# Kernel optimization log

Measured on AMD Instinct MI355X. Metric: run time of the kernel, lower is better.

Reference implementation:

```python
import jax, jax.numpy as jnp
import numpy as np

B, N, ENC, DEC, ATT = 32, 4096, 1024, 512, 512


def setup_inputs() -> dict:
    key = jax.random.key(0)
    ks = jax.random.split(key, 8)
    s_enc = 1.0 / np.sqrt(ENC)
    s_dec = 1.0 / np.sqrt(DEC)
    s_att = 1.0 / np.sqrt(ATT)
    return {
        "encoder_out": jax.random.normal(ks[0], (B, N, ENC), jnp.float32),
        "decoder_hidden": jax.random.normal(ks[1], (B, DEC), jnp.float32),
        "W_enc": jax.random.uniform(ks[2], (ENC, ATT), jnp.float32, -s_enc, s_enc),
        "b_enc": jax.random.uniform(ks[3], (ATT,), jnp.float32, -s_enc, s_enc),
        "W_dec": jax.random.uniform(ks[4], (DEC, ATT), jnp.float32, -s_dec, s_dec),
        "b_dec": jax.random.uniform(ks[5], (ATT,), jnp.float32, -s_dec, s_dec),
        "w_full": jax.random.uniform(ks[6], (ATT,), jnp.float32, -s_att, s_att),
        "b_full": jax.random.uniform(ks[7], (), jnp.float32, -s_att, s_att),
    }


def reference(encoder_out, decoder_hidden, W_enc, b_enc, W_dec, b_dec, w_full, b_full):
    # att1: [B, N, ATT]; att2: [B, 1, ATT]
    att1 = jnp.einsum('bne,ea->bna', encoder_out, W_enc) + b_enc
    att2 = (decoder_hidden @ W_dec + b_dec)[:, None, :]
    att = jax.nn.relu(att1 + att2)
    e = jnp.einsum('bna,a->bn', att, w_full) + b_full  # [B, N]
    alpha = jax.nn.softmax(e, axis=1)
    awe = jnp.einsum('bne,bn->be', encoder_out, alpha)  # weighted encoding [B, ENC]
    return awe, alpha
```

## Files before the change

kernel.cpp:

```cpp
#include <hip/hip_runtime.h>

#define B_ 32
#define N_ 4096
#define ENC_ 1024
#define DEC_ 512
#define ATT_ 512

typedef __attribute__((ext_vector_type(8))) short short8;
typedef __attribute__((ext_vector_type(4))) float f32x4;

__device__ __forceinline__ short f2bf(float f) {
  union { float f; unsigned u; } x; x.f = f;
  unsigned r = (x.u + 0x7FFFu + ((x.u >> 16) & 1u)) >> 16;
  return (short)r;
}

__device__ __forceinline__ void lds_barrier() {
  asm volatile("s_waitcnt lgkmcnt(0)" ::: "memory");
  __builtin_amdgcn_s_barrier();
  asm volatile("" ::: "memory");
}

extern "C" __global__ void __launch_bounds__(256) prep_kernel(
    const float* __restrict__ dh, const float* __restrict__ W_dec,
    const float* __restrict__ b_dec, const float* __restrict__ b_enc,
    const float* __restrict__ W_enc,
    float* __restrict__ att2, short* __restrict__ Wfrag)
{
  if (blockIdx.x < B_) {
    __shared__ float dhs[DEC_];
    int b = blockIdx.x;
    for (int i = threadIdx.x; i < DEC_; i += 256) dhs[i] = dh[b * DEC_ + i];
    __syncthreads();
    for (int a = threadIdx.x; a < ATT_; a += 256) {
      float s = b_dec[a] + b_enc[a];
      for (int k = 0; k < DEC_; ++k) s += dhs[k] * W_dec[k * ATT_ + a];
      att2[b * ATT_ + a] = s;
    }
  } else {
    int idx = (blockIdx.x - B_) * 256 + threadIdx.x;
    int l = idx & 63;
    int g = (idx >> 6) & 31;
    int c = idx >> 11;
    int col = c * 16 + (l & 15);
    int kb = g * 32 + (l >> 4) * 8;
    short8 p;
#pragma unroll
    for (int j = 0; j < 8; ++j) p[j] = f2bf(W_enc[(kb + j) * ATT_ + col]);
    *(short8*)(Wfrag + ((long)idx << 3)) = p;
  }
}

extern "C" __global__ void __launch_bounds__(256, 2) gemm_e_kernel(
    const float* __restrict__ enc, const short* __restrict__ Wfrag,
    const float* __restrict__ att2, const float* __restrict__ w_full,
    float* __restrict__ e_part)
{
  __shared__ __align__(16) short As[2][64 * 64];
  __shared__ float e_red[64][4];

  const int tid = threadIdx.x;
  const int lane = tid & 63;
  const int w = tid >> 6;
  const int blk = blockIdx.x;
  const int g16 = blk >> 4;
  const int h = (blk >> 3) & 1;
  const int p = g16 * 8 + (blk & 7);
  const int b = p >> 6;
  const int n0 = (p & 63) * 64;

  const int arow = tid >> 2;
  const int akc = tid & 3;
  const float* aptr = enc + ((long)(b * N_ + n0 + arow)) * ENC_ + akc * 16;
  const int awb0 = (arow * 128 + akc * 32) ^ ((arow & 7) << 4);
  const int awb1 = (arow * 128 + akc * 32 + 16) ^ ((arow & 7) << 4);

  int arbyte[4][2];
#pragma unroll
  for (int r = 0; r < 4; ++r) {
    int rr = r * 16 + (lane & 15);
#pragma unroll
    for (int s = 0; s < 2; ++s)
      arbyte[r][s] =
          (rr * 128 + (lane >> 4) * 16 + s * 64) ^ ((rr & 7) << 4);
  }

  const short* bptr = Wfrag + (long)(h * 16 + w * 4) * 16384 + lane * 8;

  f32x4 acc[4][4] = {};
  short8 bfgA[4], bfgB[4];
  f32x4 pA[4];

  {
    f32x4 v0 = *(const f32x4*)(aptr);
    f32x4 v1 = *(const f32x4*)(aptr + 4);
    f32x4 v2 = *(const f32x4*)(aptr + 8);
    f32x4 v3 = *(const f32x4*)(aptr + 12);
    short8 q0, q1;
#pragma unroll
    for (int j = 0; j < 4; ++j) {
      q0[j] = f2bf(v0[j]); q0[j + 4] = f2bf(v1[j]);
      q1[j] = f2bf(v2[j]); q1[j + 4] = f2bf(v3[j]);
    }
    *(short8*)((char*)As[0] + awb0) = q0;
    *(short8*)((char*)As[0] + awb1) = q1;
  }
#pragma unroll
  for (int cc = 0; cc < 4; ++cc)
    bfgA[cc] = *(const short8*)(bptr + cc * 16384);
  lds_barrier();

#pragma unroll
  for (int t = 0; t < 16; ++t) {
    const int cur = t & 1;
    if (t + 1 < 16) {
#pragma unroll
      for (int i = 0; i < 4; ++i)
        pA[i] = *(const f32x4*)(aptr + (t + 1) * 64 + i * 4);
    }
    {
#pragma unroll
      for (int cc = 0; cc < 4; ++cc)
        bfgB[cc] = *(const short8*)(bptr + cc * 16384 + (2 * t + 1) * 512);
      short8 af[4];
#pragma unroll
      for (int r = 0; r < 4; ++r)
        af[r] = *(const short8*)((const char*)As[cur] + arbyte[r][0]);
      __builtin_amdgcn_s_setprio(1);
#pragma unroll
      for (int cc = 0; cc < 4; ++cc)
#pragma unroll
        for (int r = 0; r < 4; ++r)
          acc[r][cc] = __builtin_amdgcn_mfma_f32_16x16x32_bf16(
              af[r], bfgA[cc], acc[r][cc], 0, 0, 0);
      __builtin_amdgcn_s_setprio(0);
    }
    {
      if (2 * t + 2 < 32) {
#pragma unroll
        for (int cc = 0; cc < 4; ++cc)
          bfgA[cc] = *(const short8*)(bptr + cc * 16384 + (2 * t + 2) * 512);
      }
      short8 af[4];
#pragma unroll
      for (int r = 0; r < 4; ++r)
        af[r] = *(const short8*)((const char*)As[cur] + arbyte[r][1]);
      __builtin_amdgcn_s_setprio(1);
#pragma unroll
      for (int cc = 0; cc < 4; ++cc)
#pragma unroll
        for (int r = 0; r < 4; ++r)
          acc[r][cc] = __builtin_amdgcn_mfma_f32_16x16x32_bf16(
              af[r], bfgB[cc], acc[r][cc], 0, 0, 0);
      __builtin_amdgcn_s_setprio(0);
    }
    if (t + 1 < 16) {
      short8 q0, q1;
#pragma unroll
      for (int j = 0; j < 4; ++j) {
        q0[j] = f2bf(pA[0][j]); q0[j + 4] = f2bf(pA[1][j]);
        q1[j] = f2bf(pA[2][j]); q1[j + 4] = f2bf(pA[3][j]);
      }
      *(short8*)((char*)As[cur ^ 1] + awb0) = q0;
      *(short8*)((char*)As[cur ^ 1] + awb1) = q1;
      lds_barrier();
    }
  }

  const int lq = lane >> 4, lr = lane & 15;
  float at2v[4], wv[4];
#pragma unroll
  for (int c = 0; c < 4; ++c) {
    int col = h * 256 + w * 64 + c * 16 + lr;
    at2v[c] = att2[b * ATT_ + col];
    wv[c] = w_full[col];
  }
#pragma unroll
  for (int r = 0; r < 4; ++r) {
#pragma unroll
    for (int j = 0; j < 4; ++j) {
      float s = 0.f;
#pragma unroll
      for (int c = 0; c < 4; ++c)
        s += fmaxf(acc[r][c][j] + at2v[c], 0.f) * wv[c];
      s += __shfl_xor(s, 1); s += __shfl_xor(s, 2);
      s += __shfl_xor(s, 4); s += __shfl_xor(s, 8);
      if (lr == 0) e_red[r * 16 + lq * 4 + j][w] = s;
    }
  }
  __syncthreads();
  if (tid < 64) {
    float ev = e_red[tid][0] + e_red[tid][1] + e_red[tid][2] + e_red[tid][3];
    e_part[(long)h * (B_ * N_) + b * N_ + n0 + tid] = ev;
  }
}

extern "C" __global__ void __launch_bounds__(256) softmax_kernel(
    const float* __restrict__ e, float* __restrict__ alpha)
{
  int b = blockIdx.x, tid = threadIdx.x;
  float v[16];
  float m = -1e30f;
#pragma unroll
  for (int i = 0; i < 16; ++i) {
    int idx = b * N_ + i * 256 + tid;
    v[i] = e[idx] + e[B_ * N_ + idx];
    m = fmaxf(m, v[i]);
  }
  for (int off = 1; off < 64; off <<= 1) m = fmaxf(m, __shfl_xor(m, off));
  __shared__ float redm[4];
  if ((tid & 63) == 0) redm[tid >> 6] = m;
  __syncthreads();
  m = fmaxf(fmaxf(redm[0], redm[1]), fmaxf(redm[2], redm[3]));
  float s = 0.f;
#pragma unroll
  for (int i = 0; i < 16; ++i) { v[i] = expf(v[i] - m); s += v[i]; }
  for (int off = 1; off < 64; off <<= 1) s += __shfl_xor(s, off);
  __shared__ float reds[4];
  if ((tid & 63) == 0) reds[tid >> 6] = s;
  __syncthreads();
  s = reds[0] + reds[1] + reds[2] + reds[3];
  float inv = 1.0f / s;
#pragma unroll
  for (int i = 0; i < 16; ++i) alpha[b * N_ + i * 256 + tid] = v[i] * inv;
}

extern "C" __global__ void __launch_bounds__(256) awe_part_kernel(
    const float* __restrict__ enc, const float* __restrict__ alpha,
    float* __restrict__ part)
{
  __shared__ float als[256];
  __shared__ f32x4 red[256];
  int bi = blockIdx.x;
  int b = bi & 31, cchunk = (bi >> 5) & 3, nchunk = bi >> 7;
  int t = threadIdx.x;
  int n0 = nchunk * 256;
  als[t] = alpha[b * N_ + n0 + t];
  __syncthreads();
  int tcol = t & 63, tn = t >> 6;
  const float* base = enc + (long)b * N_ * ENC_ + (long)n0 * ENC_ +
                      cchunk * 256 + tcol * 4;
  f32x4 acc = {};
  for (int i = tn; i < 256; i += 4) {
    f32x4 vv = *(const f32x4*)(base + (long)i * ENC_);
    acc += als[i] * vv;
  }
  red[t] = acc;
  __syncthreads();
  if (t < 64) {
    f32x4 s = red[t] + red[t + 64] + red[t + 128] + red[t + 192];
    *(f32x4*)(&part[(long)nchunk * 32768 + b * 1024 + cchunk * 256 + t * 4]) = s;
  }
}

extern "C" __global__ void __launch_bounds__(256) awe_reduce_kernel(
    const float* __restrict__ part, float* __restrict__ awe)
{
  int i = blockIdx.x * 256 + threadIdx.x;
  float s = 0.f;
#pragma unroll
  for (int p = 0; p < 16; ++p) s += part[(long)p * 32768 + i];
  awe[i] = s;
}

extern "C" void kernel_launch(void* const* d_in, const int* in_sizes, int n_in,
                              void* d_out, int out_size, void* d_ws, size_t ws_size,
                              hipStream_t stream) {
  const float* enc    = (const float*)d_in[0];
  const float* dh     = (const float*)d_in[1];
  const float* W_enc  = (const float*)d_in[2];
  const float* b_enc  = (const float*)d_in[3];
  const float* W_dec  = (const float*)d_in[4];
  const float* b_dec  = (const float*)d_in[5];
  const float* w_full = (const float*)d_in[6];
  float* out = (float*)d_out;

  char* ws = (char*)d_ws;
  float* att2  = (float*)ws;
  short* Wfrag = (short*)(ws + 65536);
  float* e_buf = (float*)(ws + 65536 + 1048576);
  float* part  = (float*)(ws + 65536 + 1048576 + 1048576);

  hipLaunchKernelGGL(prep_kernel, dim3(B_ + 256), dim3(256), 0, stream,
                     dh, W_dec, b_dec, b_enc, W_enc, att2, Wfrag);
  hipLaunchKernelGGL(gemm_e_kernel, dim3(4096), dim3(256), 0, stream,
                     enc, Wfrag, att2, w_full, e_buf);
  hipLaunchKernelGGL(softmax_kernel, dim3(B_), dim3(256), 0, stream,
                     e_buf, out + B_ * ENC_);
  hipLaunchKernelGGL(awe_part_kernel, dim3(2048), dim3(256), 0, stream,
                     enc, out + B_ * ENC_, part);
  hipLaunchKernelGGL(awe_reduce_kernel, dim3(128), dim3(256), 0, stream,
                     part, out);
}
```

Baseline: 328.2 us.

## Stage encoder tiles via direct global-to-LDS loads and convert to bf16 on read

Replaces the register-staged A-tile path (global load, bf16 convert, LDS store) with global_load_lds DMA of raw fp32 tiles into a swizzled LDS layout, converting to bf16 when fragments are read. It also drops the B-fragment register double-buffering, loading B per k-step instead, and raises the occupancy hint from 2 to 3 blocks per CU. The aim is to cut VGPR pressure and the instruction overhead of staging. In exchange LDS use doubles to 32 KB per buffer pair, which may limit occupancy, and conversion work is repeated on every read.

```diff
diff --git a/kernel.cpp b/kernel.cpp
--- a/kernel.cpp
+++ b/kernel.cpp
@@ -15,10 +15,10 @@
   return (short)r;
 }
 
-__device__ __forceinline__ void lds_barrier() {
-  asm volatile("s_waitcnt lgkmcnt(0)" ::: "memory");
-  __builtin_amdgcn_s_barrier();
-  asm volatile("" ::: "memory");
+__device__ __forceinline__ void gl_lds16(const float* g, void* l) {
+  __builtin_amdgcn_global_load_lds(
+      (const __attribute__((address_space(1))) unsigned int*)g,
+      (__attribute__((address_space(3))) unsigned int*)l, 16, 0, 0);
 }
 
 extern "C" __global__ void __launch_bounds__(256) prep_kernel(
@@ -51,12 +51,12 @@
   }
 }
 
-extern "C" __global__ void __launch_bounds__(256, 2) gemm_e_kernel(
+extern "C" __global__ void __launch_bounds__(256, 3) gemm_e_kernel(
     const float* __restrict__ enc, const short* __restrict__ Wfrag,
     const float* __restrict__ att2, const float* __restrict__ w_full,
     float* __restrict__ e_part)
 {
-  __shared__ __align__(16) short As[2][64 * 64];
+  __shared__ __align__(16) float As[2][64 * 64];
   __shared__ float e_red[64][4];
 
   const int tid = threadIdx.x;
@@ -69,102 +69,69 @@
   const int b = p >> 6;
   const int n0 = (p & 63) * 64;
 
-  const int arow = tid >> 2;
-  const int akc = tid & 3;
-  const float* aptr = enc + ((long)(b * N_ + n0 + arow)) * ENC_ + akc * 16;
-  const int awb0 = (arow * 128 + akc * 32) ^ ((arow & 7) << 4);
-  const int awb1 = (arow * 128 + akc * 32 + 16) ^ ((arow & 7) << 4);
-
-  int arbyte[4][2];
-#pragma unroll
-  for (int r = 0; r < 4; ++r) {
-    int rr = r * 16 + (lane & 15);
-#pragma unroll
-    for (int s = 0; s < 2; ++s)
-      arbyte[r][s] =
-          (rr * 128 + (lane >> 4) * 16 + s * 64) ^ ((rr & 7) << 4);
-  }
+  const int qv = lane >> 4;
+  const int ch = lane & 15;
+
+  const float* asrc[4];
+#pragma unroll
+  for (int j = 0; j < 4; ++j) {
+    int rl = j * 4 + qv;
+    asrc[j] = enc + (long)(b * N_ + n0 + w * 16 + rl) * ENC_ +
+              ((ch ^ ((qv + (j & 1) * 4) & 7)) << 2);
+  }
+
+  const int abase0 = ch * 256 + (((qv * 2 + 0) ^ (ch & 7)) << 4);
+  const int abase1 = ch * 256 + (((qv * 2 + 1) ^ (ch & 7)) << 4);
 
   const short* bptr = Wfrag + (long)(h * 16 + w * 4) * 16384 + lane * 8;
 
   f32x4 acc[4][4] = {};
-  short8 bfgA[4], bfgB[4];
-  f32x4 pA[4];
 
   {
-    f32x4 v0 = *(const f32x4*)(aptr);
-    f32x4 v1 = *(const f32x4*)(aptr + 4);
-    f32x4 v2 = *(const f32x4*)(aptr + 8);
-    f32x4 v3 = *(const f32x4*)(aptr + 12);
-    short8 q0, q1;
-#pragma unroll
-    for (int j = 0; j < 4; ++j) {
-      q0[j] = f2bf(v0[j]); q0[j + 4] = f2bf(v1[j]);
-      q1[j] = f2bf(v2[j]); q1[j + 4] = f2bf(v3[j]);
-    }
-    *(short8*)((char*)As[0] + awb0) = q0;
-    *(short8*)((char*)As[0] + awb1) = q1;
-  }
-#pragma unroll
-  for (int cc = 0; cc < 4; ++cc)
-    bfgA[cc] = *(const short8*)(bptr + cc * 16384);
-  lds_barrier();
+    char* d = (char*)(&As[0][0]) + (w << 12);
+#pragma unroll
+    for (int j = 0; j < 4; ++j) gl_lds16(asrc[j], d + j * 1024);
+  }
+  __syncthreads();
 
 #pragma unroll
   for (int t = 0; t < 16; ++t) {
     const int cur = t & 1;
     if (t + 1 < 16) {
-#pragma unroll
-      for (int i = 0; i < 4; ++i)
-        pA[i] = *(const f32x4*)(aptr + (t + 1) * 64 + i * 4);
-    }
-    {
+      char* d = (char*)(&As[cur ^ 1][0]) + (w << 12);
+#pragma unroll
+      for (int j = 0; j < 4; ++j)
+        gl_lds16(asrc[j] + (t + 1) * 64, d + j * 1024);
+    }
+#pragma unroll
+    for (int ks = 0; ks < 2; ++ks) {
+      short8 bfg[4];
 #pragma unroll
       for (int cc = 0; cc < 4; ++cc)
-        bfgB[cc] = *(const short8*)(bptr + cc * 16384 + (2 * t + 1) * 512);
+        bfg[cc] = *(const short8*)(bptr + cc * 16384 + (2 * t + ks) * 512);
       short8 af[4];
 #pragma unroll
-      for (int r = 0; r < 4; ++r)
-        af[r] = *(const short8*)((const char*)As[cur] + arbyte[r][0]);
+      for (int r = 0; r < 4; ++r) {
+        f32x4 lo = *(const f32x4*)((const char*)(&As[cur][0]) +
+                                   (abase0 + r * 4096 + ks * 128));
+        f32x4 hi = *(const f32x4*)((const char*)(&As[cur][0]) +
+                                   (abase1 + r * 4096 + ks * 128));
+#pragma unroll
+        for (int j = 0; j < 4; ++j) {
+          af[r][j] = f2bf(lo[j]);
+          af[r][j + 4] = f2bf(hi[j]);
+        }
+      }
       __builtin_amdgcn_s_setprio(1);
 #pragma unroll
       for (int cc = 0; cc < 4; ++cc)
 #pragma unroll
         for (int r = 0; r < 4; ++r)
           acc[r][cc] = __builtin_amdgcn_mfma_f32_16x16x32_bf16(
-              af[r], bfgA[cc], acc[r][cc], 0, 0, 0);
+              af[r], bfg[cc], acc[r][cc], 0, 0, 0);
       __builtin_amdgcn_s_setprio(0);
     }
-    {
-      if (2 * t + 2 < 32) {
-#pragma unroll
-        for (int cc = 0; cc < 4; ++cc)
-          bfgA[cc] = *(const short8*)(bptr + cc * 16384 + (2 * t + 2) * 512);
-      }
-      short8 af[4];
-#pragma unroll
-      for (int r = 0; r < 4; ++r)
-        af[r] = *(const short8*)((const char*)As[cur] + arbyte[r][1]);
-      __builtin_amdgcn_s_setprio(1);
-#pragma unroll
-      for (int cc = 0; cc < 4; ++cc)
-#pragma unroll
-        for (int r = 0; r < 4; ++r)
-          acc[r][cc] = __builtin_amdgcn_mfma_f32_16x16x32_bf16(
-              af[r], bfgB[cc], acc[r][cc], 0, 0, 0);
-      __builtin_amdgcn_s_setprio(0);
-    }
-    if (t + 1 < 16) {
-      short8 q0, q1;
-#pragma unroll
-      for (int j = 0; j < 4; ++j) {
-        q0[j] = f2bf(pA[0][j]); q0[j + 4] = f2bf(pA[1][j]);
-        q1[j] = f2bf(pA[2][j]); q1[j + 4] = f2bf(pA[3][j]);
-      }
-      *(short8*)((char*)As[cur ^ 1] + awb0) = q0;
-      *(short8*)((char*)As[cur ^ 1] + awb1) = q1;
-      lds_barrier();
-    }
+    __syncthreads();
   }
 
   const int lq = lane >> 4, lr = lane & 15;
```

Result: slower. 356.2 us (+8.5%).

## Restructure GEMM main loop with explicit vmcnt waits and hardware bf16 pack conversion

Applied to the files above, without the earlier changes.

Reorders the per-step loads so that both B fragment groups are issued first, then the next A tile. sched_barriers and explicit s_waitcnt vmcnt counts gate each MFMA half on only the loads it needs. The software round-to-nearest bf16 conversion is replaced with the v_cvt_pk_bf16_f32 instruction, and launch bounds ask for 3 blocks per CU. The aim is to cut conversion ALU work and improve load/MFMA overlap. Costs are a removed cross-iteration B prefetch, a barrier on every iteration, and register pressure from the occupancy hint, which may cause spills.

```diff
diff --git a/kernel.cpp b/kernel.cpp
--- a/kernel.cpp
+++ b/kernel.cpp
@@ -8,12 +8,23 @@
 
 typedef __attribute__((ext_vector_type(8))) short short8;
 typedef __attribute__((ext_vector_type(4))) float f32x4;
+typedef __attribute__((ext_vector_type(4))) unsigned u32x4;
 
 __device__ __forceinline__ short f2bf(float f) {
   union { float f; unsigned u; } x; x.f = f;
   unsigned r = (x.u + 0x7FFFu + ((x.u >> 16) & 1u)) >> 16;
   return (short)r;
 }
+
+__device__ __forceinline__ unsigned cvtpk(float a, float b) {
+  unsigned r;
+  asm("v_cvt_pk_bf16_f32 %0, %1, %2" : "=v"(r) : "v"(a), "v"(b));
+  return r;
+}
+
+#define VMCNT(N)                                            \
+  asm volatile("s_waitcnt vmcnt(" #N ")" ::: "memory");     \
+  __builtin_amdgcn_sched_barrier(0)
 
 __device__ __forceinline__ void lds_barrier() {
   asm volatile("s_waitcnt lgkmcnt(0)" ::: "memory");
@@ -51,7 +62,7 @@
   }
 }
 
-extern "C" __global__ void __launch_bounds__(256, 2) gemm_e_kernel(
+extern "C" __global__ void __launch_bounds__(256, 3) gemm_e_kernel(
     const float* __restrict__ enc, const short* __restrict__ Wfrag,
     const float* __restrict__ att2, const float* __restrict__ w_full,
     float* __restrict__ e_part)
@@ -88,83 +99,85 @@
   const short* bptr = Wfrag + (long)(h * 16 + w * 4) * 16384 + lane * 8;
 
   f32x4 acc[4][4] = {};
-  short8 bfgA[4], bfgB[4];
   f32x4 pA[4];
 
+  pA[0] = *(const f32x4*)(aptr);
+  pA[1] = *(const f32x4*)(aptr + 4);
+  pA[2] = *(const f32x4*)(aptr + 8);
+  pA[3] = *(const f32x4*)(aptr + 12);
   {
-    f32x4 v0 = *(const f32x4*)(aptr);
-    f32x4 v1 = *(const f32x4*)(aptr + 4);
-    f32x4 v2 = *(const f32x4*)(aptr + 8);
-    f32x4 v3 = *(const f32x4*)(aptr + 12);
-    short8 q0, q1;
-#pragma unroll
-    for (int j = 0; j < 4; ++j) {
-      q0[j] = f2bf(v0[j]); q0[j + 4] = f2bf(v1[j]);
-      q1[j] = f2bf(v2[j]); q1[j + 4] = f2bf(v3[j]);
-    }
-    *(short8*)((char*)As[0] + awb0) = q0;
-    *(short8*)((char*)As[0] + awb1) = q1;
-  }
-#pragma unroll
-  for (int cc = 0; cc < 4; ++cc)
-    bfgA[cc] = *(const short8*)(bptr + cc * 16384);
+    union { u32x4 u; short8 s; } q0, q1;
+    q0.u[0] = cvtpk(pA[0][0], pA[0][1]); q0.u[1] = cvtpk(pA[0][2], pA[0][3]);
+    q0.u[2] = cvtpk(pA[1][0], pA[1][1]); q0.u[3] = cvtpk(pA[1][2], pA[1][3]);
+    q1.u[0] = cvtpk(pA[2][0], pA[2][1]); q1.u[1] = cvtpk(pA[2][2], pA[2][3]);
+    q1.u[2] = cvtpk(pA[3][0], pA[3][1]); q1.u[3] = cvtpk(pA[3][2], pA[3][3]);
+    *(short8*)((char*)As[0] + awb0) = q0.s;
+    *(short8*)((char*)As[0] + awb1) = q1.s;
+  }
   lds_barrier();
 
 #pragma unroll
   for (int t = 0; t < 16; ++t) {
     const int cur = t & 1;
+
+    short8 bfg[8];
+#pragma unroll
+    for (int cc = 0; cc < 4; ++cc)
+      bfg[cc] = *(const short8*)(bptr + cc * 16384 + (2 * t) * 512);
+#pragma unroll
+    for (int cc = 0; cc < 4; ++cc)
+      bfg[4 + cc] = *(const short8*)(bptr + cc * 16384 + (2 * t + 1) * 512);
+    __builtin_amdgcn_sched_barrier(0);
     if (t + 1 < 16) {
-#pragma unroll
-      for (int i = 0; i < 4; ++i)
-        pA[i] = *(const f32x4*)(aptr + (t + 1) * 64 + i * 4);
-    }
+      const float* ap = aptr + (t + 1) * 64;
+      pA[0] = *(const f32x4*)(ap);
+      pA[1] = *(const f32x4*)(ap + 4);
+      pA[2] = *(const f32x4*)(ap + 8);
+      pA[3] = *(const f32x4*)(ap + 12);
+    }
+    __builtin_amdgcn_sched_barrier(0);
+
     {
-#pragma unroll
-      for (int cc = 0; cc < 4; ++cc)
-        bfgB[cc] = *(const short8*)(bptr + cc * 16384 + (2 * t + 1) * 512);
       short8 af[4];
 #pragma unroll
       for (int r = 0; r < 4; ++r)
         af[r] = *(const short8*)((const char*)As[cur] + arbyte[r][0]);
+      VMCNT(8);
       __builtin_amdgcn_s_setprio(1);
 #pragma unroll
       for (int cc = 0; cc < 4; ++cc)
 #pragma unroll
         for (int r = 0; r < 4; ++r)
           acc[r][cc] = __builtin_amdgcn_mfma_f32_16x16x32_bf16(
-              af[r], bfgA[cc], acc[r][cc], 0, 0, 0);
+              af[r], bfg[cc], acc[r][cc], 0, 0, 0);
       __builtin_amdgcn_s_setprio(0);
     }
     {
-      if (2 * t + 2 < 32) {
-#pragma unroll
-        for (int cc = 0; cc < 4; ++cc)
-          bfgA[cc] = *(const short8*)(bptr + cc * 16384 + (2 * t + 2) * 512);
-      }
       short8 af[4];
 #pragma unroll
       for (int r = 0; r < 4; ++r)
         af[r] = *(const short8*)((const char*)As[cur] + arbyte[r][1]);
+      VMCNT(4);
       __builtin_amdgcn_s_setprio(1);
 #pragma unroll
       for (int cc = 0; cc < 4; ++cc)
 #pragma unroll
         for (int r = 0; r < 4; ++r)
           acc[r][cc] = __builtin_amdgcn_mfma_f32_16x16x32_bf16(
-              af[r], bfgB[cc], acc[r][cc], 0, 0, 0);
+              af[r], bfg[4 + cc], acc[r][cc], 0, 0, 0);
       __builtin_amdgcn_s_setprio(0);
     }
     if (t + 1 < 16) {
-      short8 q0, q1;
-#pragma unroll
-      for (int j = 0; j < 4; ++j) {
-        q0[j] = f2bf(pA[0][j]); q0[j + 4] = f2bf(pA[1][j]);
-        q1[j] = f2bf(pA[2][j]); q1[j + 4] = f2bf(pA[3][j]);
-      }
-      *(short8*)((char*)As[cur ^ 1] + awb0) = q0;
-      *(short8*)((char*)As[cur ^ 1] + awb1) = q1;
-      lds_barrier();
-    }
+      VMCNT(0);
+      union { u32x4 u; short8 s; } q0, q1;
+      q0.u[0] = cvtpk(pA[0][0], pA[0][1]); q0.u[1] = cvtpk(pA[0][2], pA[0][3]);
+      q0.u[2] = cvtpk(pA[1][0], pA[1][1]); q0.u[3] = cvtpk(pA[1][2], pA[1][3]);
+      q1.u[0] = cvtpk(pA[2][0], pA[2][1]); q1.u[1] = cvtpk(pA[2][2], pA[2][3]);
+      q1.u[2] = cvtpk(pA[3][0], pA[3][1]); q1.u[3] = cvtpk(pA[3][2], pA[3][3]);
+      *(short8*)((char*)As[cur ^ 1] + awb0) = q0.s;
+      *(short8*)((char*)As[cur ^ 1] + awb1) = q1.s;
+    }
+    lds_barrier();
   }
 
   const int lq = lane >> 4, lr = lane & 15;
```

Result: no change. 332.4 us (+1.3%).
